# Kernel tuning notes

Measured on AMD Instinct MI355X. Metric: run time of the kernel, lower is better.

Reference implementation:

```python
import jax, jax.numpy as jnp
import numpy as np

B = 65536
HID = 256
C_K, C_V, C_S, NQ = 4, 8, 4, 4
EMB_OUT = 64  # state_embedding_size - 1


def _spatial_basis():
    # h = w = 5, U = V = 2 -> [5,5,4] Fourier basis
    ph = jnp.arange(1.0, 6.0)[:, None] * jnp.ones((1, 5)) * (np.pi / 5.0)
    pw = jnp.ones((5, 1)) * jnp.arange(1.0, 6.0)[None, :] * (np.pi / 5.0)
    u = jnp.arange(1.0, 3.0)[None, :]
    a = jnp.cos(ph[:, :, None] * u)  # [5,5,2]
    b = jnp.cos(pw[:, :, None] * u)  # [5,5,2]
    return jnp.einsum('hwu,hwv->hwuv', a, b).reshape(5, 5, 4).astype(jnp.float32)


def _conv(x, w, b):
    # x: NHWC, w: HWIO, pad=1, stride=1
    y = jax.lax.conv_general_dilated(x, w, window_strides=(1, 1), padding=[(1, 1), (1, 1)],
                                     dimension_numbers=('NHWC', 'HWIO', 'NHWC'))
    return y + b


def setup_inputs() -> dict:
    key = jax.random.key(0)
    ks = jax.random.split(key, 20)
    s = 0.05
    inp = {
        'X': jax.random.normal(ks[0], (B, 7, 7, 3), jnp.float32),
        'upper_module_hidden_state': jax.random.normal(ks[1], (B, HID), jnp.float32),
        'c1_w': jax.random.normal(ks[2], (5, 5, 3, 8), jnp.float32) * s,
        'c1_b': jax.random.normal(ks[3], (8,), jnp.float32) * s,
        'c2_w': jax.random.normal(ks[4], (3, 3, 8, 12), jnp.float32) * s,
        'c2_b': jax.random.normal(ks[5], (12,), jnp.float32) * s,
    }
    qdims = [(HID, 256), (256, 128), (128, 64), (64, 32), (32, 32)]
    for i, (din, dout) in enumerate(qdims):
        inp[f'qw{i}'] = jax.random.normal(ks[6 + 2 * i], (din, dout), jnp.float32) * s
        inp[f'qb{i}'] = jax.random.normal(ks[7 + 2 * i], (dout,), jnp.float32) * s
    inp['aw0'] = jax.random.normal(ks[16], ((C_V + C_S) * NQ, 32), jnp.float32) * s
    inp['ab0'] = jax.random.normal(ks[17], (32,), jnp.float32) * s
    inp['aw1'] = jax.random.normal(ks[18], (32, EMB_OUT), jnp.float32) * s
    inp['ab1'] = jax.random.normal(ks[19], (EMB_OUT,), jnp.float32) * s
    return inp


def reference(X, upper_module_hidden_state, c1_w, c1_b, c2_w, c2_b,
              qw0, qb0, qw1, qb1, qw2, qb2, qw3, qb3, qw4, qb4,
              aw0, ab0, aw1, ab1):
    b = X.shape[0]
    # vision CNN: [b,7,7,3] -> [b,5,5,8] -> [b,5,5,12]
    O = _conv(_conv(X, c1_w, c1_b), c2_w, c2_b)
    K, V = O[..., :C_K], O[..., C_K:]
    S = jnp.broadcast_to(_spatial_basis(), (b, 5, 5, C_S))
    K = jnp.concatenate([K, S], axis=-1)  # [b,5,5,8]
    V = jnp.concatenate([V, S], axis=-1)  # [b,5,5,12]
    # query MLP -> [b,4,8]
    q = upper_module_hidden_state
    for w, bi in [(qw0, qb0), (qw1, qb1), (qw2, qb2), (qw3, qb3)]:
        q = jax.nn.relu(q @ w + bi)
    q = (q @ qw4 + qb4).reshape(-1, NQ, C_K + C_S)
    # attention logits over 25 spatial positions, softmax over space
    A = jnp.einsum('bhwk,bqk->bhwq', K, q).reshape(b, 25, NQ)
    A = jax.nn.softmax(A, axis=1)
    # apply_alpha: [b,nq,25] @ [b,25,12] -> [b,nq,12]; chunk+cat == reshape
    a = jnp.einsum('bpq,bpd->bqd', A, V.reshape(b, 25, C_V + C_S)).reshape(b, NQ * (C_V + C_S))
    # answer MLP
    return jax.nn.relu(a @ aw0 + ab0) @ aw1 + ab1
```

## Files before the change

kernel.cpp:

```cpp
#include <hip/hip_runtime.h>
#include <hip/hip_bf16.h>

#define NB 65536

typedef __attribute__((ext_vector_type(8))) short short8;
typedef __attribute__((ext_vector_type(4))) short short4v;
typedef __attribute__((ext_vector_type(4))) float f32x4;
typedef __attribute__((ext_vector_type(16))) float f32x16;
typedef __attribute__((ext_vector_type(4))) unsigned int u32x4;

__device__ inline short f2bf(float f) {
    unsigned u = __builtin_bit_cast(unsigned, f);
    unsigned r = (u + 0x7fffu + ((u >> 16) & 1u)) >> 16;
    return (short)(unsigned short)r;
}
__device__ inline float b2f(short s) {
    return __builtin_bit_cast(float, (unsigned)((unsigned short)s) << 16);
}
__device__ inline unsigned pkbf(float lo, float hi) {
    return ((unsigned)(unsigned short)f2bf(hi) << 16) | (unsigned)(unsigned short)f2bf(lo);
}

#define MLPW_CNT 109568
#define WEFF_CNT 51200
#define A0 (MLPW_CNT + WEFF_CNT + 320)
#define A1 (A0 + 2048)
#define A2 (A1 + 2048)
#define A3 (A2 + 100)
#define PREP_TOT (A3 + 512)

__global__ void __launch_bounds__(256) prep_kernel(
    const float* __restrict__ w0, const float* __restrict__ w1,
    const float* __restrict__ w2, const float* __restrict__ w3,
    const float* __restrict__ w4,
    const float* __restrict__ b0, const float* __restrict__ b1,
    const float* __restrict__ b2, const float* __restrict__ b3,
    const float* __restrict__ b4,
    const float* __restrict__ c1w, const float* __restrict__ c1b,
    const float* __restrict__ c2w, const float* __restrict__ c2b,
    const float* __restrict__ aw0, const float* __restrict__ aw1,
    short* __restrict__ wt, short* __restrict__ weff, float* __restrict__ beff,
    short* __restrict__ aw0T, short* __restrict__ aw1T, float* __restrict__ sTab,
    float* __restrict__ biasP)
{
    int idx = blockIdx.x * 256 + threadIdx.x;
    if (idx < MLPW_CNT) {
        const float* W; int N, KT, base;
        if (idx < 65536)       { W = w0; N = 256; KT = 16; base = 0; }
        else if (idx < 98304)  { W = w1; N = 128; KT = 16; base = 65536; }
        else if (idx < 106496) { W = w2; N = 64;  KT = 8;  base = 98304; }
        else if (idx < 108544) { W = w3; N = 32;  KT = 4;  base = 106496; }
        else                   { W = w4; N = 32;  KT = 2;  base = 108544; }
        int i  = idx - base;
        int nt = i / (KT * 512);
        int r1 = i - nt * (KT * 512);
        int kt = r1 >> 9;
        int l  = (r1 & 511) >> 3;
        int j  = i & 7;
        int n  = nt * 32 + (l & 31);
        int k  = kt * 16 + ((l >> 5) << 3) + j;
        wt[idx] = f2bf(W[k * N + n]);
    } else if (idx < MLPW_CNT + WEFF_CNT) {
        int it = idx - MLPW_CNT;
        int n = it / 160, k = it - n * 160;
        float acc = 0.f;
        if (n < 300 && k < 147) {
            int oc = n % 12, p = n / 12, oy = p / 5, ox = p - oy * 5;
            int ci = k % 3,  t = k / 3, iy = t / 7, ix = t - iy * 7;
            for (int y = 0; y < 5; ++y) {
                int ky = iy - y + 1, ly = y - oy + 1;
                if ((unsigned)ky < 5u && (unsigned)ly < 3u) {
                    for (int x = 0; x < 5; ++x) {
                        int kx = ix - x + 1, lx = x - ox + 1;
                        if ((unsigned)kx < 5u && (unsigned)lx < 3u) {
                            const float* p1 = c1w + ((ky * 5 + kx) * 3 + ci) * 8;
                            const float* p2 = c2w + ((ly * 3 + lx) * 8) * 12 + oc;
#pragma unroll
                            for (int c = 0; c < 8; ++c) acc += p1[c] * p2[c * 12];
                        }
                    }
                }
            }
        }
        weff[it] = f2bf(acc);
    } else if (idx < A0) {
        int n = idx - MLPW_CNT - WEFF_CNT;
        float acc = 0.f;
        if (n < 300) {
            int oc = n % 12, p = n / 12, oy = p / 5, ox = p - oy * 5;
            acc = c2b[oc];
            for (int y = 0; y < 5; ++y) {
                int ly = y - oy + 1;
                if ((unsigned)ly < 3u) {
                    for (int x = 0; x < 5; ++x) {
                        int lx = x - ox + 1;
                        if ((unsigned)lx < 3u) {
#pragma unroll
                            for (int c = 0; c < 8; ++c)
                                acc += c2w[((ly * 3 + lx) * 8 + c) * 12 + oc] * c1b[c];
                        }
                    }
                }
            }
        }
        beff[n] = acc;
    } else if (idx < A1) {
        int t = idx - A0;
        int n = t >> 6, k = t & 63;
        aw0T[t] = (k < 48) ? f2bf(aw0[k * 32 + n]) : (short)0;
    } else if (idx < A2) {
        int t = idx - A1;
        int n = t >> 5, k = t & 31;
        aw1T[t] = f2bf(aw1[k * 64 + n]);
    } else if (idx < A3) {
        int i = idx - A2;
        int p = i >> 2, s = i & 3;
        int h = p / 5, w = p - 5 * h;
        int u = (s >> 1) + 1, v = (s & 1) + 1;
        const float PI5 = 0.6283185307179586f;
        sTab[i] = cosf(((float)(h + 1) * PI5) * (float)u) *
                  cosf(((float)(w + 1) * PI5) * (float)v);
    } else if (idx < PREP_TOT) {
        int t = idx - A3;
        const float* B; int N, base;
        if (t < 256)      { B = b0; N = 256; base = 0; }
        else if (t < 384) { B = b1; N = 128; base = 256; }
        else if (t < 448) { B = b2; N = 64;  base = 384; }
        else if (t < 480) { B = b3; N = 32;  base = 448; }
        else              { B = b4; N = 32;  base = 480; }
        int u  = t - base;
        int h  = u / (N / 2);
        int w  = u - h * (N / 2);
        int nt = w >> 4, r = w & 15;
        biasP[t] = B[nt * 32 + (r & 3) + 8 * (r >> 2) + 4 * h];
    }
}

template<int KT, int THREADS>
__device__ inline void stage_load(const short* __restrict__ src,
                                  short8* r, int tid)
{
    constexpr int CNT = (KT * 64 + THREADS - 1) / THREADS;
#pragma unroll
    for (int i = 0; i < CNT; ++i) {
        int idx = tid + i * THREADS;
        if (idx < KT * 64) r[i] = *(const short8*)(src + idx * 8);
    }
}
template<int KT, int THREADS>
__device__ inline void stage_write(short* __restrict__ dst,
                                   const short8* r, int tid)
{
    constexpr int CNT = (KT * 64 + THREADS - 1) / THREADS;
#pragma unroll
    for (int i = 0; i < CNT; ++i) {
        int idx = tid + i * THREADS;
        if (idx < KT * 64) *(short8*)(dst + idx * 8) = r[i];
    }
}

template<int K, int N, bool RELU, int THREADS>
__device__ inline void layerS(const short* __restrict__ wp,
                              const float* __restrict__ bp,
                              const u32x4* __restrict__ inF,
                              u32x4* __restrict__ outF,
                              short* __restrict__ sW0,
                              short* __restrict__ sW1,
                              int tid, int lane, int h)
{
    constexpr int KT = K / 16, NT = N / 32;
    constexpr int CNT = (KT * 64 + THREADS - 1) / THREADS;
    short8 tmp[CNT];

    stage_load<KT, THREADS>(wp, tmp, tid);
    stage_write<KT, THREADS>(sW0, tmp, tid);
    __syncthreads();

#pragma unroll
    for (int nt = 0; nt < NT; ++nt) {
        short* cur = (nt & 1) ? sW1 : sW0;
        short* nxt = (nt & 1) ? sW0 : sW1;
        if (nt + 1 < NT) stage_load<KT, THREADS>(wp + (nt + 1) * KT * 512, tmp, tid);

        f32x16 a;
#pragma unroll
        for (int r = 0; r < 16; ++r) a[r] = 0.f;
#pragma unroll
        for (int kt = 0; kt < KT; ++kt) {
            short8 wf = *(const short8*)(cur + kt * 512 + lane * 8);
            a = __builtin_amdgcn_mfma_f32_32x32x16_bf16(
                    wf, __builtin_bit_cast(short8, inF[kt]), a, 0, 0, 0);
        }
        const float* bpp = bp + h * (N / 2) + nt * 16;
        unsigned q[8];
#pragma unroll
        for (int i = 0; i < 8; ++i) {
            float v0 = a[2 * i] + bpp[2 * i];
            float v1 = a[2 * i + 1] + bpp[2 * i + 1];
            if (RELU) { v0 = fmaxf(v0, 0.f); v1 = fmaxf(v1, 0.f); }
            q[i] = pkbf(v0, v1);
        }
        unsigned xq[8];
#pragma unroll
        for (int i = 0; i < 8; ++i) xq[i] = (unsigned)__shfl_xor((int)q[i], 32, 64);
        u32x4 fa, fb;
        if (h == 0) {
            fa[0] = q[0];  fa[1] = q[1];  fa[2] = xq[0]; fa[3] = xq[1];
            fb[0] = q[4];  fb[1] = q[5];  fb[2] = xq[4]; fb[3] = xq[5];
        } else {
            fa[0] = xq[2]; fa[1] = xq[3]; fa[2] = q[2];  fa[3] = q[3];
            fb[0] = xq[6]; fb[1] = xq[7]; fb[2] = q[6];  fb[3] = q[7];
        }
        outF[2 * nt]     = fa;
        outF[2 * nt + 1] = fb;

        if (nt + 1 < NT) stage_write<KT, THREADS>(nxt, tmp, tid);
        __syncthreads();
    }
}

template<int K>
__device__ inline void layerQ(const short* __restrict__ wp,
                              const float* __restrict__ bp,
                              const u32x4* __restrict__ inF,
                              short* __restrict__ qout,
                              int lane, int h, int r0)
{
    constexpr int KT = K / 16;
    f32x16 a;
#pragma unroll
    for (int r = 0; r < 16; ++r) a[r] = 0.f;
#pragma unroll
    for (int kt = 0; kt < KT; ++kt) {
        short8 wf = *(const short8*)(wp + kt * 512 + lane * 8);
        a = __builtin_amdgcn_mfma_f32_32x32x16_bf16(
                wf, __builtin_bit_cast(short8, inF[kt]), a, 0, 0, 0);
    }
    const float* bpp = bp + h * 16;
    short* qb = qout + (size_t)(r0 + (lane & 31)) * 32 + 4 * h;
    const int fo[8] = {0, 2, 8, 10, 16, 18, 24, 26};
#pragma unroll
    for (int i = 0; i < 8; ++i) {
        float v0 = a[2 * i] + bpp[2 * i];
        float v1 = a[2 * i + 1] + bpp[2 * i + 1];
        *(unsigned*)(qb + fo[i]) = pkbf(v0, v1);
    }
}

__global__ void __launch_bounds__(512, 1) mlp_kernel(
    const float* __restrict__ hid,
    const short* __restrict__ wp,
    const float* __restrict__ biasP,
    short* __restrict__ qout)
{
    __shared__ __align__(16) short sW0[8192];
    __shared__ __align__(16) short sW1[8192];

    const int tid  = threadIdx.x;
    const int lane = tid & 63;
    const int wv   = tid >> 6;
    const int h = lane >> 5, b = lane & 31;
    const int r0 = blockIdx.x * 256 + wv * 32;

    u32x4 A[16], B[16], C[8], D[4], E[2];
    const float* hb = hid + (size_t)(r0 + b) * 256 + h * 8;
#pragma unroll
    for (int kt = 0; kt < 16; ++kt) {
        float4 x = *(const float4*)(hb + kt * 16);
        float4 y = *(const float4*)(hb + kt * 16 + 4);
        u32x4 f;
        f[0] = pkbf(x.x, x.y); f[1] = pkbf(x.z, x.w);
        f[2] = pkbf(y.x, y.y); f[3] = pkbf(y.z, y.w);
        A[kt] = f;
    }
    layerS<256, 256, true, 512>(wp,          biasP,       A, B, sW0, sW1, tid, lane, h);
    layerS<256, 128, true, 512>(wp + 65536,  biasP + 256, B, C, sW0, sW1, tid, lane, h);
    layerS<128,  64, true, 512>(wp + 98304,  biasP + 384, C, D, sW0, sW1, tid, lane, h);
    layerS< 64,  32, true, 512>(wp + 106496, biasP + 448, D, E, sW0, sW1, tid, lane, h);
    layerQ< 32>                (wp + 108544, biasP + 480, E, qout, lane, h, r0);
}

typedef __attribute__((address_space(1))) const void glb_v;
typedef __attribute__((address_space(3))) void lds_v;

__global__ void __launch_bounds__(256, 3) conv_attn_kernel(
    const float* __restrict__ Xg,
    const short* __restrict__ weffT,
    const float* __restrict__ beff,
    const short* __restrict__ aw0T, const float* __restrict__ ab0,
    const short* __restrict__ aw1T, const float* __restrict__ ab1,
    const float* __restrict__ sTab,
    const short* __restrict__ qb16,
    float* __restrict__ out)
{
    __shared__ __align__(16) short sPool[4][4800];
    __shared__ __align__(16) short sB[2][2560];

    const int tid    = threadIdx.x;
    const int w      = tid >> 6;
    const int lane   = tid & 63;
    const int lanelo = lane & 15;
    const int g      = lane >> 4;
    const int e0     = blockIdx.x * 64 + w * 16;

    short* sKc = &sPool[w][0];
    short* sVc = &sPool[w][1600];
    short* sAh = &sPool[w][0];
    short* sHh = &sPool[w][1024];

    const int elq = lane >> 2, qiq = lane & 3;
    short8 qv = *(const short8*)(qb16 + (size_t)(e0 + elq) * 32 + qiq * 8);

    short8 af[5];
    {
        const float* xr = Xg + (size_t)(e0 + lanelo) * 147;
        const int c0g = g * 8;
#pragma unroll
        for (int kt = 0; kt < 5; ++kt) {
            int c0 = kt * 32 + c0g;
            float v[8];
#pragma unroll
            for (int j = 0; j < 8; ++j) {
                int c = c0 + j;
                v[j] = (c < 147) ? xr[c] : 0.f;
            }
            u32x4 u;
            u[0] = pkbf(v[0], v[1]); u[1] = pkbf(v[2], v[3]);
            u[2] = pkbf(v[4], v[5]); u[3] = pkbf(v[6], v[7]);
            af[kt] = __builtin_bit_cast(short8, u);
        }
    }

    float bv[19];
#pragma unroll
    for (int nt = 0; nt < 19; ++nt) bv[nt] = beff[nt * 16 + lanelo];

#define STAGE_B(NT_, BUF_)                                                     \
    {                                                                          \
        const short* src0 = weffT + ((NT_) * 16 + lanelo) * 160 + w * 32 + g * 8; \
        __builtin_amdgcn_global_load_lds((glb_v*)src0,                         \
            (lds_v*)(&sB[BUF_][w * 512]), 16, 0, 0);                           \
        if (w == 0) {                                                          \
            const short* src1 = weffT + ((NT_) * 16 + lanelo) * 160 + 4 * 32 + g * 8; \
            __builtin_amdgcn_global_load_lds((glb_v*)src1,                     \
                (lds_v*)(&sB[BUF_][4 * 512]), 16, 0, 0);                       \
        }                                                                      \
    }

    STAGE_B(0, 0)
    __syncthreads();

#pragma unroll
    for (int nt = 0; nt < 19; ++nt) {
        const int cur = nt & 1;
        if (nt + 1 < 19) {
            if ((nt & 1) == 0) { STAGE_B(nt + 1, 1) }
            else               { STAGE_B(nt + 1, 0) }
        }
        f32x4 a; a[0] = 0.f; a[1] = 0.f; a[2] = 0.f; a[3] = 0.f;
#pragma unroll
        for (int kt = 0; kt < 5; ++kt) {
            short8 bfv = *(const short8*)(&sB[cur][kt * 512 + lane * 8]);
            a = __builtin_amdgcn_mfma_f32_16x16x32_bf16(af[kt], bfv, a, 0, 0, 0);
        }
        int n = nt * 16 + lanelo;
        if (n < 300) {
            int p = n / 12, c = n - p * 12;
#pragma unroll
            for (int j = 0; j < 4; ++j) {
                int el = g * 4 + j;
                float v = a[j] + bv[nt];
                if (c < 4) sKc[el * 100 + p * 4 + c]       = f2bf(v);
                else       sVc[el * 200 + p * 8 + (c - 4)] = f2bf(v);
            }
        }
        __syncthreads();
    }
#undef STAGE_B

    {
        const int el = elq, qi = qiq;
        float qf[8];
#pragma unroll
        for (int i = 0; i < 8; ++i) qf[i] = b2f(qv[i]);

        float lg[25];
        float mx = -1e30f;
#pragma unroll
        for (int c = 0; c < 5; ++c) {
            short4v kv[5]; float4 sv[5];
#pragma unroll
            for (int i = 0; i < 5; ++i) {
                int p = c * 5 + i;
                kv[i] = *(const short4v*)(sKc + el * 100 + p * 4);
                sv[i] = *(const float4*)(sTab + p * 4);
            }
#pragma unroll
            for (int i = 0; i < 5; ++i) {
                float s = b2f(kv[i][0]) * qf[0] + b2f(kv[i][1]) * qf[1]
                        + b2f(kv[i][2]) * qf[2] + b2f(kv[i][3]) * qf[3]
                        + sv[i].x * qf[4] + sv[i].y * qf[5]
                        + sv[i].z * qf[6] + sv[i].w * qf[7];
                lg[c * 5 + i] = s;
                mx = fmaxf(mx, s);
            }
        }
        float sum = 0.f;
#pragma unroll
        for (int p = 0; p < 25; ++p) { lg[p] = __expf(lg[p] - mx); sum += lg[p]; }
        float inv = 1.f / sum;

        float o[12];
#pragma unroll
        for (int d = 0; d < 12; ++d) o[d] = 0.f;
#pragma unroll
        for (int c = 0; c < 5; ++c) {
            short4v v0[5], v1[5]; float4 sv[5];
#pragma unroll
            for (int i = 0; i < 5; ++i) {
                int p = c * 5 + i;
                v0[i] = *(const short4v*)(sVc + el * 200 + p * 8);
                v1[i] = *(const short4v*)(sVc + el * 200 + p * 8 + 4);
                sv[i] = *(const float4*)(sTab + p * 4);
            }
#pragma unroll
            for (int i = 0; i < 5; ++i) {
                float wgt = lg[c * 5 + i];
                o[0] += wgt * b2f(v0[i][0]); o[1] += wgt * b2f(v0[i][1]);
                o[2] += wgt * b2f(v0[i][2]); o[3] += wgt * b2f(v0[i][3]);
                o[4] += wgt * b2f(v1[i][0]); o[5] += wgt * b2f(v1[i][1]);
                o[6] += wgt * b2f(v1[i][2]); o[7] += wgt * b2f(v1[i][3]);
                o[8]  += wgt * sv[i].x; o[9]  += wgt * sv[i].y;
                o[10] += wgt * sv[i].z; o[11] += wgt * sv[i].w;
            }
        }
#pragma unroll
        for (int d = 0; d < 12; ++d) {
            int col = qi * 12 + d;
            int ch = col >> 3;
            sAh[el * 64 + ((ch ^ (el & 7)) << 3) + (col & 7)] = f2bf(o[d] * inv);
        }
#pragma unroll
        for (int z = 0; z < 4; ++z) {
            int col = 48 + qi * 4 + z;
            int ch = col >> 3;
            sAh[el * 64 + ((ch ^ (el & 7)) << 3) + (col & 7)] = 0;
        }
    }

    {
        short8 bw0a = *(const short8*)(aw0T + (0 * 16 + lanelo) * 64 + g * 8);
        short8 bw1a = *(const short8*)(aw0T + (0 * 16 + lanelo) * 64 + 32 + g * 8);
        short8 bw0b = *(const short8*)(aw0T + (1 * 16 + lanelo) * 64 + g * 8);
        short8 bw1b = *(const short8*)(aw0T + (1 * 16 + lanelo) * 64 + 32 + g * 8);
        float bba = ab0[lanelo];
        float bbb = ab0[16 + lanelo];

        short8 aa0, aa1;
        {
            int p0 = (0 * 4 + g) ^ (lanelo & 7);
            int p1 = (1 * 4 + g) ^ (lanelo & 7);
            aa0 = *(const short8*)(sAh + lanelo * 64 + p0 * 8);
            aa1 = *(const short8*)(sAh + lanelo * 64 + p1 * 8);
        }
        f32x4 h0; h0[0] = 0.f; h0[1] = 0.f; h0[2] = 0.f; h0[3] = 0.f;
        f32x4 h1 = h0;
        h0 = __builtin_amdgcn_mfma_f32_16x16x32_bf16(aa0, bw0a, h0, 0, 0, 0);
        h0 = __builtin_amdgcn_mfma_f32_16x16x32_bf16(aa1, bw1a, h0, 0, 0, 0);
        h1 = __builtin_amdgcn_mfma_f32_16x16x32_bf16(aa0, bw0b, h1, 0, 0, 0);
        h1 = __builtin_amdgcn_mfma_f32_16x16x32_bf16(aa1, bw1b, h1, 0, 0, 0);
#pragma unroll
        for (int j = 0; j < 4; ++j) {
            int row = g * 4 + j;
            int n0 = lanelo, n1 = 16 + lanelo;
            float va = fmaxf(h0[j] + bba, 0.f);
            float vb = fmaxf(h1[j] + bbb, 0.f);
            sHh[row * 32 + (((n0 >> 3) ^ (row & 3)) << 3) + (n0 & 7)] = f2bf(va);
            sHh[row * 32 + (((n1 >> 3) ^ (row & 3)) << 3) + (n1 & 7)] = f2bf(vb);
        }
    }

    {
        short8 bw[4]; float bb[4];
#pragma unroll
        for (int nt3 = 0; nt3 < 4; ++nt3) {
            int n = nt3 * 16 + lanelo;
            bw[nt3] = *(const short8*)(aw1T + n * 32 + g * 8);
            bb[nt3] = ab1[n];
        }
        short8 ah;
        {
            int ph = (g ^ (lanelo & 3));
            ah = *(const short8*)(sHh + lanelo * 32 + ph * 8);
        }
#pragma unroll
        for (int nt3 = 0; nt3 < 4; ++nt3) {
            int n = nt3 * 16 + lanelo;
            f32x4 oacc; oacc[0] = 0.f; oacc[1] = 0.f; oacc[2] = 0.f; oacc[3] = 0.f;
            oacc = __builtin_amdgcn_mfma_f32_16x16x32_bf16(ah, bw[nt3], oacc, 0, 0, 0);
#pragma unroll
            for (int j = 0; j < 4; ++j) {
                int el = g * 4 + j;
                out[((size_t)e0 + el) * 64 + n] = oacc[j] + bb[nt3];
            }
        }
    }
}


extern "C" void kernel_launch(void* const* d_in, const int* in_sizes, int n_in,
                              void* d_out, int out_size, void* d_ws, size_t ws_size,
                              hipStream_t stream)
{
    const float* X   = (const float*)d_in[0];
    const float* hid = (const float*)d_in[1];
    const float* c1w = (const float*)d_in[2];
    const float* c1b = (const float*)d_in[3];
    const float* c2w = (const float*)d_in[4];
    const float* c2b = (const float*)d_in[5];
    const float* qw0 = (const float*)d_in[6];
    const float* qb0 = (const float*)d_in[7];
    const float* qw1 = (const float*)d_in[8];
    const float* qb1 = (const float*)d_in[9];
    const float* qw2 = (const float*)d_in[10];
    const float* qb2 = (const float*)d_in[11];
    const float* qw3 = (const float*)d_in[12];
    const float* qb3 = (const float*)d_in[13];
    const float* qw4 = (const float*)d_in[14];
    const float* qb4 = (const float*)d_in[15];
    const float* aw0 = (const float*)d_in[16];
    const float* ab0 = (const float*)d_in[17];
    const float* aw1 = (const float*)d_in[18];
    const float* ab1 = (const float*)d_in[19];

    float* out   = (float*)d_out;
    short* qb16  = (short*)d_ws;
    short* wsW   = qb16 + (size_t)NB * 32;
    short* weffT = wsW + MLPW_CNT;
    float* beff  = (float*)(weffT + WEFF_CNT);
    short* aw0T  = (short*)(beff + 320);
    short* aw1T  = aw0T + 2048;
    float* sTab  = (float*)(aw1T + 2048);
    float* biasP = sTab + 100;

    hipLaunchKernelGGL(prep_kernel, dim3((PREP_TOT + 255) / 256), dim3(256), 0, stream,
                       qw0, qw1, qw2, qw3, qw4, qb0, qb1, qb2, qb3, qb4,
                       c1w, c1b, c2w, c2b, aw0, aw1,
                       wsW, weffT, beff, aw0T, aw1T, sTab, biasP);
    hipLaunchKernelGGL(mlp_kernel, dim3(NB / 256), dim3(512), 0, stream,
                       hid, wsW, biasP, qb16);
    hipLaunchKernelGGL(conv_attn_kernel, dim3(NB / 64), dim3(256), 0, stream,
                       X, weffT, beff, aw0T, ab0, aw1T, ab1, sTab, qb16, out);
}
```

Measured before the change: 72.60 us.

## Load conv weights directly to registers and process two tiles per block

The shared-LDS double-buffered weight staging, with a block-wide barrier after each of the 19 column tiles, is replaced by per-wave register prefetch of the effective conv weights from global/L2 in a 3-deep rotation. The barriers go away, since each wave now only touches its own LDS slice. Each block also loops over two 64-element tiles, halving the grid, and launch bounds drop to 2 blocks per CU. The cost is higher register pressure and more global/L2 weight traffic, since every wave reloads the full weight matrix for each tile. Occupancy may also fall.

```diff
diff --git a/kernel.cpp b/kernel.cpp
--- a/kernel.cpp
+++ b/kernel.cpp
@@ -280,10 +280,7 @@
     layerQ< 32>                (wp + 108544, biasP + 480, E, qout, lane, h, r0);
 }
 
-typedef __attribute__((address_space(1))) const void glb_v;
-typedef __attribute__((address_space(3))) void lds_v;
-
-__global__ void __launch_bounds__(256, 3) conv_attn_kernel(
+__global__ void __launch_bounds__(256, 2) conv_attn_kernel(
     const float* __restrict__ Xg,
     const short* __restrict__ weffT,
     const float* __restrict__ beff,
@@ -294,14 +291,12 @@
     float* __restrict__ out)
 {
     __shared__ __align__(16) short sPool[4][4800];
-    __shared__ __align__(16) short sB[2][2560];
 
     const int tid    = threadIdx.x;
     const int w      = tid >> 6;
     const int lane   = tid & 63;
     const int lanelo = lane & 15;
     const int g      = lane >> 4;
-    const int e0     = blockIdx.x * 64 + w * 16;
 
     short* sKc = &sPool[w][0];
     short* sVc = &sPool[w][1600];
@@ -309,199 +304,196 @@
     short* sHh = &sPool[w][1024];
 
     const int elq = lane >> 2, qiq = lane & 3;
-    short8 qv = *(const short8*)(qb16 + (size_t)(e0 + elq) * 32 + qiq * 8);
-
-    short8 af[5];
-    {
-        const float* xr = Xg + (size_t)(e0 + lanelo) * 147;
-        const int c0g = g * 8;
-#pragma unroll
-        for (int kt = 0; kt < 5; ++kt) {
-            int c0 = kt * 32 + c0g;
-            float v[8];
-#pragma unroll
-            for (int j = 0; j < 8; ++j) {
-                int c = c0 + j;
-                v[j] = (c < 147) ? xr[c] : 0.f;
-            }
-            u32x4 u;
-            u[0] = pkbf(v[0], v[1]); u[1] = pkbf(v[2], v[3]);
-            u[2] = pkbf(v[4], v[5]); u[3] = pkbf(v[6], v[7]);
-            af[kt] = __builtin_bit_cast(short8, u);
-        }
-    }
 
     float bv[19];
 #pragma unroll
     for (int nt = 0; nt < 19; ++nt) bv[nt] = beff[nt * 16 + lanelo];
 
-#define STAGE_B(NT_, BUF_)                                                     \
-    {                                                                          \
-        const short* src0 = weffT + ((NT_) * 16 + lanelo) * 160 + w * 32 + g * 8; \
-        __builtin_amdgcn_global_load_lds((glb_v*)src0,                         \
-            (lds_v*)(&sB[BUF_][w * 512]), 16, 0, 0);                           \
-        if (w == 0) {                                                          \
-            const short* src1 = weffT + ((NT_) * 16 + lanelo) * 160 + 4 * 32 + g * 8; \
-            __builtin_amdgcn_global_load_lds((glb_v*)src1,                     \
-                (lds_v*)(&sB[BUF_][4 * 512]), 16, 0, 0);                       \
-        }                                                                      \
-    }
-
-    STAGE_B(0, 0)
-    __syncthreads();
-
-#pragma unroll
-    for (int nt = 0; nt < 19; ++nt) {
-        const int cur = nt & 1;
-        if (nt + 1 < 19) {
-            if ((nt & 1) == 0) { STAGE_B(nt + 1, 1) }
-            else               { STAGE_B(nt + 1, 0) }
-        }
-        f32x4 a; a[0] = 0.f; a[1] = 0.f; a[2] = 0.f; a[3] = 0.f;
-#pragma unroll
-        for (int kt = 0; kt < 5; ++kt) {
-            short8 bfv = *(const short8*)(&sB[cur][kt * 512 + lane * 8]);
-            a = __builtin_amdgcn_mfma_f32_16x16x32_bf16(af[kt], bfv, a, 0, 0, 0);
-        }
-        int n = nt * 16 + lanelo;
-        if (n < 300) {
-            int p = n / 12, c = n - p * 12;
+    for (int t = 0; t < 2; ++t) {
+        const int e0 = blockIdx.x * 128 + t * 64 + w * 16;
+
+        short8 qv = *(const short8*)(qb16 + (size_t)(e0 + elq) * 32 + qiq * 8);
+
+        short8 af[5];
+        {
+            const float* xr = Xg + (size_t)(e0 + lanelo) * 147;
+            const int c0g = g * 8;
+#pragma unroll
+            for (int kt = 0; kt < 5; ++kt) {
+                int c0 = kt * 32 + c0g;
+                float v[8];
+#pragma unroll
+                for (int j = 0; j < 8; ++j) {
+                    int c = c0 + j;
+                    v[j] = (c < 147) ? xr[c] : 0.f;
+                }
+                u32x4 u;
+                u[0] = pkbf(v[0], v[1]); u[1] = pkbf(v[2], v[3]);
+                u[2] = pkbf(v[4], v[5]); u[3] = pkbf(v[6], v[7]);
+                af[kt] = __builtin_bit_cast(short8, u);
+            }
+        }
+
+        short8 bf[3][5];
+        {
+            const short* wb0 = weffT + lanelo * 160 + g * 8;
+            const short* wb1 = weffT + (16 + lanelo) * 160 + g * 8;
+#pragma unroll
+            for (int kt = 0; kt < 5; ++kt) {
+                bf[0][kt] = *(const short8*)(wb0 + kt * 32);
+                bf[1][kt] = *(const short8*)(wb1 + kt * 32);
+            }
+        }
+#pragma unroll
+        for (int nt = 0; nt < 19; ++nt) {
+            if (nt + 2 < 19) {
+                const short* wb = weffT + ((nt + 2) * 16 + lanelo) * 160 + g * 8;
+#pragma unroll
+                for (int kt = 0; kt < 5; ++kt)
+                    bf[(nt + 2) % 3][kt] = *(const short8*)(wb + kt * 32);
+            }
+            f32x4 a; a[0] = 0.f; a[1] = 0.f; a[2] = 0.f; a[3] = 0.f;
+#pragma unroll
+            for (int kt = 0; kt < 5; ++kt)
+                a = __builtin_amdgcn_mfma_f32_16x16x32_bf16(af[kt], bf[nt % 3][kt], a, 0, 0, 0);
+            int n = nt * 16 + lanelo;
+            if (n < 300) {
+                int p = n / 12, c = n - p * 12;
+#pragma unroll
+                for (int j = 0; j < 4; ++j) {
+                    int el = g * 4 + j;
+                    float v = a[j] + bv[nt];
+                    if (c < 4) sKc[el * 100 + p * 4 + c]       = f2bf(v);
+                    else       sVc[el * 200 + p * 8 + (c - 4)] = f2bf(v);
+                }
+            }
+        }
+
+        {
+            const int el = elq, qi = qiq;
+            float qf[8];
+#pragma unroll
+            for (int i = 0; i < 8; ++i) qf[i] = b2f(qv[i]);
+
+            float lg[25];
+            float mx = -1e30f;
+#pragma unroll
+            for (int c = 0; c < 5; ++c) {
+                short4v kv[5]; float4 sv[5];
+#pragma unroll
+                for (int i = 0; i < 5; ++i) {
+                    int p = c * 5 + i;
+                    kv[i] = *(const short4v*)(sKc + el * 100 + p * 4);
+                    sv[i] = *(const float4*)(sTab + p * 4);
+                }
+#pragma unroll
+                for (int i = 0; i < 5; ++i) {
+                    float s = b2f(kv[i][0]) * qf[0] + b2f(kv[i][1]) * qf[1]
+                            + b2f(kv[i][2]) * qf[2] + b2f(kv[i][3]) * qf[3]
+                            + sv[i].x * qf[4] + sv[i].y * qf[5]
+                            + sv[i].z * qf[6] + sv[i].w * qf[7];
+                    lg[c * 5 + i] = s;
+                    mx = fmaxf(mx, s);
+                }
+            }
+            float sum = 0.f;
+#pragma unroll
+            for (int p = 0; p < 25; ++p) { lg[p] = __expf(lg[p] - mx); sum += lg[p]; }
+            float inv = 1.f / sum;
+
+            float o[12];
+#pragma unroll
+            for (int d = 0; d < 12; ++d) o[d] = 0.f;
+#pragma unroll
+            for (int c = 0; c < 5; ++c) {
+                short4v v0[5], v1[5]; float4 sv[5];
+#pragma unroll
+                for (int i = 0; i < 5; ++i) {
+                    int p = c * 5 + i;
+                    v0[i] = *(const short4v*)(sVc + el * 200 + p * 8);
+                    v1[i] = *(const short4v*)(sVc + el * 200 + p * 8 + 4);
+                    sv[i] = *(const float4*)(sTab + p * 4);
+                }
+#pragma unroll
+                for (int i = 0; i < 5; ++i) {
+                    float wgt = lg[c * 5 + i];
+                    o[0] += wgt * b2f(v0[i][0]); o[1] += wgt * b2f(v0[i][1]);
+                    o[2] += wgt * b2f(v0[i][2]); o[3] += wgt * b2f(v0[i][3]);
+                    o[4] += wgt * b2f(v1[i][0]); o[5] += wgt * b2f(v1[i][1]);
+                    o[6] += wgt * b2f(v1[i][2]); o[7] += wgt * b2f(v1[i][3]);
+                    o[8]  += wgt * sv[i].x; o[9]  += wgt * sv[i].y;
+                    o[10] += wgt * sv[i].z; o[11] += wgt * sv[i].w;
+                }
+            }
+#pragma unroll
+            for (int d = 0; d < 12; ++d) {
+                int col = qi * 12 + d;
+                int ch = col >> 3;
+                sAh[el * 64 + ((ch ^ (el & 7)) << 3) + (col & 7)] = f2bf(o[d] * inv);
+            }
+#pragma unroll
+            for (int z = 0; z < 4; ++z) {
+                int col = 48 + qi * 4 + z;
+                int ch = col >> 3;
+                sAh[el * 64 + ((ch ^ (el & 7)) << 3) + (col & 7)] = 0;
+            }
+        }
+
+        {
+            short8 bw0a = *(const short8*)(aw0T + (0 * 16 + lanelo) * 64 + g * 8);
+            short8 bw1a = *(const short8*)(aw0T + (0 * 16 + lanelo) * 64 + 32 + g * 8);
+            short8 bw0b = *(const short8*)(aw0T + (1 * 16 + lanelo) * 64 + g * 8);
+            short8 bw1b = *(const short8*)(aw0T + (1 * 16 + lanelo) * 64 + 32 + g * 8);
+            float bba = ab0[lanelo];
+            float bbb = ab0[16 + lanelo];
+
+            short8 aa0, aa1;
+            {
+                int p0 = (0 * 4 + g) ^ (lanelo & 7);
+                int p1 = (1 * 4 + g) ^ (lanelo & 7);
+                aa0 = *(const short8*)(sAh + lanelo * 64 + p0 * 8);
+                aa1 = *(const short8*)(sAh + lanelo * 64 + p1 * 8);
+            }
+            f32x4 h0; h0[0] = 0.f; h0[1] = 0.f; h0[2] = 0.f; h0[3] = 0.f;
+            f32x4 h1 = h0;
+            h0 = __builtin_amdgcn_mfma_f32_16x16x32_bf16(aa0, bw0a, h0, 0, 0, 0);
+            h0 = __builtin_amdgcn_mfma_f32_16x16x32_bf16(aa1, bw1a, h0, 0, 0, 0);
+            h1 = __builtin_amdgcn_mfma_f32_16x16x32_bf16(aa0, bw0b, h1, 0, 0, 0);
+            h1 = __builtin_amdgcn_mfma_f32_16x16x32_bf16(aa1, bw1b, h1, 0, 0, 0);
 #pragma unroll
             for (int j = 0; j < 4; ++j) {
-                int el = g * 4 + j;
-                float v = a[j] + bv[nt];
-                if (c < 4) sKc[el * 100 + p * 4 + c]       = f2bf(v);
-                else       sVc[el * 200 + p * 8 + (c - 4)] = f2bf(v);
-            }
-        }
-        __syncthreads();
-    }
-#undef STAGE_B
-
-    {
-        const int el = elq, qi = qiq;
-        float qf[8];
-#pragma unroll
-        for (int i = 0; i < 8; ++i) qf[i] = b2f(qv[i]);
-
-        float lg[25];
-        float mx = -1e30f;
-#pragma unroll
-        for (int c = 0; c < 5; ++c) {
-            short4v kv[5]; float4 sv[5];
-#pragma unroll
-            for (int i = 0; i < 5; ++i) {
-                int p = c * 5 + i;
-                kv[i] = *(const short4v*)(sKc + el * 100 + p * 4);
-                sv[i] = *(const float4*)(sTab + p * 4);
-            }
-#pragma unroll
-            for (int i = 0; i < 5; ++i) {
-                float s = b2f(kv[i][0]) * qf[0] + b2f(kv[i][1]) * qf[1]
-                        + b2f(kv[i][2]) * qf[2] + b2f(kv[i][3]) * qf[3]
-                        + sv[i].x * qf[4] + sv[i].y * qf[5]
-                        + sv[i].z * qf[6] + sv[i].w * qf[7];
-                lg[c * 5 + i] = s;
-                mx = fmaxf(mx, s);
-            }
-        }
-        float sum = 0.f;
-#pragma unroll
-        for (int p = 0; p < 25; ++p) { lg[p] = __expf(lg[p] - mx); sum += lg[p]; }
-        float inv = 1.f / sum;
-
-        float o[12];
-#pragma unroll
-        for (int d = 0; d < 12; ++d) o[d] = 0.f;
-#pragma unroll
-        for (int c = 0; c < 5; ++c) {
-            short4v v0[5], v1[5]; float4 sv[5];
-#pragma unroll
-            for (int i = 0; i < 5; ++i) {
-                int p = c * 5 + i;
-                v0[i] = *(const short4v*)(sVc + el * 200 + p * 8);
-                v1[i] = *(const short4v*)(sVc + el * 200 + p * 8 + 4);
-                sv[i] = *(const float4*)(sTab + p * 4);
-            }
-#pragma unroll
-            for (int i = 0; i < 5; ++i) {
-                float wgt = lg[c * 5 + i];
-                o[0] += wgt * b2f(v0[i][0]); o[1] += wgt * b2f(v0[i][1]);
-                o[2] += wgt * b2f(v0[i][2]); o[3] += wgt * b2f(v0[i][3]);
-                o[4] += wgt * b2f(v1[i][0]); o[5] += wgt * b2f(v1[i][1]);
-                o[6] += wgt * b2f(v1[i][2]); o[7] += wgt * b2f(v1[i][3]);
-                o[8]  += wgt * sv[i].x; o[9]  += wgt * sv[i].y;
-                o[10] += wgt * sv[i].z; o[11] += wgt * sv[i].w;
-            }
-        }
-#pragma unroll
-        for (int d = 0; d < 12; ++d) {
-            int col = qi * 12 + d;
-            int ch = col >> 3;
-            sAh[el * 64 + ((ch ^ (el & 7)) << 3) + (col & 7)] = f2bf(o[d] * inv);
-        }
-#pragma unroll
-        for (int z = 0; z < 4; ++z) {
-            int col = 48 + qi * 4 + z;
-            int ch = col >> 3;
-            sAh[el * 64 + ((ch ^ (el & 7)) << 3) + (col & 7)] = 0;
-        }
-    }
-
-    {
-        short8 bw0a = *(const short8*)(aw0T + (0 * 16 + lanelo) * 64 + g * 8);
-        short8 bw1a = *(const short8*)(aw0T + (0 * 16 + lanelo) * 64 + 32 + g * 8);
-        short8 bw0b = *(const short8*)(aw0T + (1 * 16 + lanelo) * 64 + g * 8);
-        short8 bw1b = *(const short8*)(aw0T + (1 * 16 + lanelo) * 64 + 32 + g * 8);
-        float bba = ab0[lanelo];
-        float bbb = ab0[16 + lanelo];
-
-        short8 aa0, aa1;
+                int row = g * 4 + j;
+                int n0 = lanelo, n1 = 16 + lanelo;
+                float va = fmaxf(h0[j] + bba, 0.f);
+                float vb = fmaxf(h1[j] + bbb, 0.f);
+                sHh[row * 32 + (((n0 >> 3) ^ (row & 3)) << 3) + (n0 & 7)] = f2bf(va);
+                sHh[row * 32 + (((n1 >> 3) ^ (row & 3)) << 3) + (n1 & 7)] = f2bf(vb);
+            }
+        }
+
         {
-            int p0 = (0 * 4 + g) ^ (lanelo & 7);
-            int p1 = (1 * 4 + g) ^ (lanelo & 7);
-            aa0 = *(const short8*)(sAh + lanelo * 64 + p0 * 8);
-            aa1 = *(const short8*)(sAh + lanelo * 64 + p1 * 8);
-        }
-        f32x4 h0; h0[0] = 0.f; h0[1] = 0.f; h0[2] = 0.f; h0[3] = 0.f;
-        f32x4 h1 = h0;
-        h0 = __builtin_amdgcn_mfma_f32_16x16x32_bf16(aa0, bw0a, h0, 0, 0, 0);
-        h0 = __builtin_amdgcn_mfma_f32_16x16x32_bf16(aa1, bw1a, h0, 0, 0, 0);
-        h1 = __builtin_amdgcn_mfma_f32_16x16x32_bf16(aa0, bw0b, h1, 0, 0, 0);
-        h1 = __builtin_amdgcn_mfma_f32_16x16x32_bf16(aa1, bw1b, h1, 0, 0, 0);
-#pragma unroll
-        for (int j = 0; j < 4; ++j) {
-            int row = g * 4 + j;
-            int n0 = lanelo, n1 = 16 + lanelo;
-            float va = fmaxf(h0[j] + bba, 0.f);
-            float vb = fmaxf(h1[j] + bbb, 0.f);
-            sHh[row * 32 + (((n0 >> 3) ^ (row & 3)) << 3) + (n0 & 7)] = f2bf(va);
-            sHh[row * 32 + (((n1 >> 3) ^ (row & 3)) << 3) + (n1 & 7)] = f2bf(vb);
-        }
-    }
-
-    {
-        short8 bw[4]; float bb[4];
-#pragma unroll
-        for (int nt3 = 0; nt3 < 4; ++nt3) {
-            int n = nt3 * 16 + lanelo;
-            bw[nt3] = *(const short8*)(aw1T + n * 32 + g * 8);
-            bb[nt3] = ab1[n];
-        }
-        short8 ah;
-        {
-            int ph = (g ^ (lanelo & 3));
-            ah = *(const short8*)(sHh + lanelo * 32 + ph * 8);
-        }
-#pragma unroll
-        for (int nt3 = 0; nt3 < 4; ++nt3) {
-            int n = nt3 * 16 + lanelo;
-            f32x4 oacc; oacc[0] = 0.f; oacc[1] = 0.f; oacc[2] = 0.f; oacc[3] = 0.f;
-            oacc = __builtin_amdgcn_mfma_f32_16x16x32_bf16(ah, bw[nt3], oacc, 0, 0, 0);
-#pragma unroll
-            for (int j = 0; j < 4; ++j) {
-                int el = g * 4 + j;
-                out[((size_t)e0 + el) * 64 + n] = oacc[j] + bb[nt3];
+            short8 bw[4]; float bb[4];
+#pragma unroll
+            for (int nt3 = 0; nt3 < 4; ++nt3) {
+                int n = nt3 * 16 + lanelo;
+                bw[nt3] = *(const short8*)(aw1T + n * 32 + g * 8);
+                bb[nt3] = ab1[n];
+            }
+            short8 ah;
+            {
+                int ph = (g ^ (lanelo & 3));
+                ah = *(const short8*)(sHh + lanelo * 32 + ph * 8);
+            }
+#pragma unroll
+            for (int nt3 = 0; nt3 < 4; ++nt3) {
+                int n = nt3 * 16 + lanelo;
+                f32x4 oacc; oacc[0] = 0.f; oacc[1] = 0.f; oacc[2] = 0.f; oacc[3] = 0.f;
+                oacc = __builtin_amdgcn_mfma_f32_16x16x32_bf16(ah, bw[nt3], oacc, 0, 0, 0);
+#pragma unroll
+                for (int j = 0; j < 4; ++j) {
+                    int el = g * 4 + j;
+                    out[((size_t)e0 + el) * 64 + n] = oacc[j] + bb[nt3];
+                }
             }
         }
     }
@@ -549,6 +541,6 @@
                        wsW, weffT, beff, aw0T, aw1T, sTab, biasP);
     hipLaunchKernelGGL(mlp_kernel, dim3(NB / 256), dim3(512), 0, stream,
                        hid, wsW, biasP, qb16);
-    hipLaunchKernelGGL(conv_attn_kernel, dim3(NB / 64), dim3(256), 0, stream,
+    hipLaunchKernelGGL(conv_attn_kernel, dim3(NB / 128), dim3(256), 0, stream,
                        X, weffT, beff, aw0T, ab0, aw1T, ab1, sTab, qb16, out);
 }
```

Measured after the change: 173.8 us. 2.39x slower.
